# Optimization experiments

Hardware: AMD Instinct MI355X
Metric: run time of the kernel (lower is better)

Reference implementation:

```python
import jax, jax.numpy as jnp
from jax import lax
import numpy as np

B, H, W, C = 2, 128, 128, 256
HEADS, DH = 8, 32
HD = HEADS * DH  # must equal C (pos_emb reshape constraint)


def _lrelu(t):
    return jnp.where(t > 0, t, 0.01 * t)


def _mlp(t, w1, b1, w2):
    # Linear(dim->hd, bias) -> LeakyReLU -> Linear(hd->hd, no bias)
    return _lrelu(t @ w1.T + b1) @ w2.T


def _dwconv(t, w, b):
    # depthwise 3x3, padding 1; t: NCHW, w: (C,1,3,3)
    o = lax.conv_general_dilated(t, w, (1, 1), ((1, 1), (1, 1)),
                                 dimension_numbers=('NCHW', 'OIHW', 'NCHW'),
                                 feature_group_count=t.shape[1])
    return o + b[None, :, None, None]


def setup_inputs():
    key = jax.random.key(0)
    ks = iter(jax.random.split(key, 48))
    def nrm(shape, s=0.02):
        return jax.random.normal(next(ks), shape, jnp.float32) * s
    inp = {
        'x_in': jax.random.normal(next(ks), (B, H, W, C), jnp.float32),
        'y_in': jax.random.normal(next(ks), (B, H, W, C), jnp.float32),
        # fusion_x / fusion_y: two 1x1 convs (stored as (out,in) matrices)
        'fx_w1': nrm((C, 2 * C)), 'fx_b1': jnp.zeros((C,), jnp.float32),
        'fx_w2': nrm((C, C)),     'fx_b2': jnp.zeros((C,), jnp.float32),
        'fy_w1': nrm((C, 2 * C)), 'fy_b1': jnp.zeros((C,), jnp.float32),
        'fy_w2': nrm((C, C)),     'fy_b2': jnp.zeros((C,), jnp.float32),
        # to_q / to_k / to_v: Linear(C->HD,+b) -> LeakyReLU -> Linear(HD->HD, no b)
        'q_w1': nrm((HD, C)), 'q_b1': jnp.zeros((HD,), jnp.float32), 'q_w2': nrm((HD, HD)),
        'k_w1': nrm((HD, C)), 'k_b1': jnp.zeros((HD,), jnp.float32), 'k_w2': nrm((HD, HD)),
        'v_w1': nrm((HD, C)), 'v_b1': jnp.zeros((HD,), jnp.float32), 'v_w2': nrm((HD, HD)),
        'rescale_x': jnp.ones((HEADS, 1, 1), jnp.float32),
        'rescale_y': jnp.ones((HEADS, 1, 1), jnp.float32),
        'px_w': nrm((C, HD)), 'px_b': jnp.zeros((C,), jnp.float32),
        'py_w': nrm((C, HD)), 'py_b': jnp.zeros((C,), jnp.float32),
        # pos_emb: two depthwise 3x3 convs with GELU between
        'pe_w1': nrm((C, 1, 3, 3)), 'pe_b1': jnp.zeros((C,), jnp.float32),
        'pe_w2': nrm((C, 1, 3, 3)), 'pe_b2': jnp.zeros((C,), jnp.float32),
    }
    return inp


def reference(x_in, y_in, fx_w1, fx_b1, fx_w2, fx_b2, fy_w1, fy_b1, fy_w2, fy_b2,
              q_w1, q_b1, q_w2, k_w1, k_b1, k_w2, v_w1, v_b1, v_w2,
              rescale_x, rescale_y, px_w, px_b, py_w, py_b,
              pe_w1, pe_b1, pe_w2, pe_b2):
    b, h, w, c = x_in.shape
    n = h * w

    xy = jnp.concatenate([x_in, y_in], axis=-1)  # (b,h,w,2c)
    fk_x = _lrelu(jnp.einsum('bhwi,oi->bhwo', xy, fx_w1) + fx_b1)
    fk_x = (jnp.einsum('bhwi,oi->bhwo', fk_x, fx_w2) + fx_b2).reshape(b, n, c)
    fk_y = _lrelu(jnp.einsum('bhwi,oi->bhwo', xy, fy_w1) + fy_b1)
    fk_y = (jnp.einsum('bhwi,oi->bhwo', fk_y, fy_w2) + fy_b2).reshape(b, n, c)

    x = x_in.reshape(b, n, c)
    y = y_in.reshape(b, n, c)
    q_inp_x = _mlp(x, q_w1, q_b1, q_w2)
    k_inp_x = _mlp(fk_x, k_w1, k_b1, k_w2)
    v_inp_x = _mlp(x, v_w1, v_b1, v_w2)
    q_inp_y = _mlp(y, q_w1, q_b1, q_w2)
    k_inp_y = _mlp(fk_y, k_w1, k_b1, k_w2)
    v_inp_y = _mlp(y, v_w1, v_b1, v_w2)

    def split_heads(t):  # (b,n,hd) -> (b,heads,d,n)  (already transposed)
        return t.reshape(b, n, HEADS, DH).transpose(0, 2, 3, 1)

    def l2n(t):
        return t / jnp.maximum(jnp.linalg.norm(t, axis=-1, keepdims=True), 1e-12)

    q_x, k_x, v_x = split_heads(q_inp_x), split_heads(k_inp_x), split_heads(v_inp_x)
    q_y, k_y, v_y = split_heads(q_inp_y), split_heads(k_inp_y), split_heads(v_inp_y)
    q_x, k_x, q_y, k_y = l2n(q_x), l2n(k_x), l2n(q_y), l2n(k_y)

    def pos_emb(v_inp):
        t = v_inp.reshape(b, h, w, c).transpose(0, 3, 1, 2)  # NCHW
        t = _dwconv(t, pe_w1, pe_b1)
        t = jax.nn.gelu(t, approximate=False)
        t = _dwconv(t, pe_w2, pe_b2)
        return t.transpose(0, 2, 3, 1)  # NHWC

    # channel (transposed) cross-attention: d x d maps per head
    attn_x = jax.nn.softmax(jnp.einsum('bhdn,bhen->bhde', k_y, q_x) * rescale_x, axis=-1)
    xo = jnp.einsum('bhde,bhen->bhdn', attn_x, v_x).transpose(0, 3, 1, 2).reshape(b, n, HD)
    out_x = (xo @ px_w.T + px_b).reshape(b, h, w, c) + pos_emb(v_inp_x)

    attn_y = jax.nn.softmax(jnp.einsum('bhdn,bhen->bhde', k_x, q_y) * rescale_y, axis=-1)
    yo = jnp.einsum('bhde,bhen->bhdn', attn_y, v_y).transpose(0, 3, 1, 2).reshape(b, n, HD)
    out_y = (yo @ py_w.T + py_b).reshape(b, h, w, c) + pos_emb(v_inp_y)

    return out_x, out_y
```

## Files before the change

kernel.cpp:

```cpp
#include <hip/hip_runtime.h>
#include <hip/hip_bf16.h>

typedef __hip_bfloat16 bf16;
typedef __attribute__((ext_vector_type(8))) short short8;
typedef __attribute__((ext_vector_type(4))) short short4v;
typedef __attribute__((ext_vector_type(4))) float f32x4;

static __device__ __forceinline__ float bfbits2f(short s) {
    return __uint_as_float(((unsigned int)(unsigned short)s) << 16);
}
static __device__ __forceinline__ float bf2f(bf16 v) { return __bfloat162float(v); }
static __device__ __forceinline__ bf16 f2bf(float v) { return __float2bfloat16(v); }
static __device__ __forceinline__ short f2bfbits(float f) {
    bf16 h = __float2bfloat16(f);
    return *reinterpret_cast<short*>(&h);
}

__launch_bounds__(256)
__global__ void cvt_xy_kernel(const float* __restrict__ x, const float* __restrict__ y,
                              bf16* __restrict__ xb, bf16* __restrict__ yb)
{
    int t = blockIdx.x * 256 + threadIdx.x;
    int which = t >> 20;
    size_t i = (size_t)(t & 1048575) * 8;
    const float4* s = (const float4*)((which ? y : x) + i);
    float4 a = s[0], b = s[1];
    short8 p;
    p[0] = f2bfbits(a.x); p[1] = f2bfbits(a.y); p[2] = f2bfbits(a.z); p[3] = f2bfbits(a.w);
    p[4] = f2bfbits(b.x); p[5] = f2bfbits(b.y); p[6] = f2bfbits(b.z); p[7] = f2bfbits(b.w);
    *(short8*)((which ? yb : xb) + i) = p;
}

struct WTab {
    const float* src[10];
    bf16* dst[10];
    int nblk[10];
};

__launch_bounds__(256)
__global__ void cvt_w_kernel(WTab tab)
{
    int b = blockIdx.x;
    int a = 0, base = 0;
    while (a < 9 && b >= base + tab.nblk[a]) { base += tab.nblk[a]; ++a; }
    int lb = b - base;
    size_t i = ((size_t)lb * 256 + threadIdx.x) * 4;
    const float4 v = *(const float4*)(tab.src[a] + i);
    bf16* d = tab.dst[a] + i;
    d[0] = f2bf(v.x); d[1] = f2bf(v.y); d[2] = f2bf(v.z); d[3] = f2bf(v.w);
}

__launch_bounds__(256)
__global__ void cvt_pe_kernel(const float* __restrict__ w1, const float* __restrict__ w2,
                              float* __restrict__ t1, float* __restrict__ t2)
{
    int t = blockIdx.x * 256 + threadIdx.x;
    if (t >= 4608) return;
    int which = t >= 2304;
    int i = which ? t - 2304 : t;
    int c = i / 9, k = i % 9;
    (which ? t2 : t1)[k * 256 + c] = (which ? w2 : w1)[i];
}

template<int ROWS>
static __device__ __forceinline__ void stage8(const bf16* __restrict__ g, int ldk,
                                              char* dst, int tid, long r0, int k0)
{
#pragma unroll
    for (int r = 0; r < ROWS / 128; ++r) {
        int row = r * 128 + (tid >> 2);
        int q = (tid & 3) * 16;
        int srcq = q ^ (((row >> 1) & 3) << 4);
        const char* gsrc = (const char*)(g + (size_t)(r0 + row) * ldk + k0) + srcq;
        char* ldst = dst + r * 8192 + ((tid >> 6) << 10);
        __builtin_amdgcn_global_load_lds(
            (const __attribute__((address_space(1))) unsigned int*)gsrc,
            (__attribute__((address_space(3))) unsigned int*)ldst, 16, 0, 0);
    }
}

static __device__ __forceinline__ int h_off(int r, int c)
{
    return ((r * 264 + c) * 2) ^ (((r >> 2) & 3) << 4);
}

template<int K1, bool CONCAT, bool STAGE2, bool B2, bool TRANSOUT, bool PROJ>
__launch_bounds__(512)
__global__ void mlp_kernel(const bf16* __restrict__ A0, const bf16* __restrict__ A1,
                           const bf16* __restrict__ B1, const float* __restrict__ b1,
                           const bf16* __restrict__ W2, const float* __restrict__ b2v,
                           bf16* __restrict__ outb, bf16* __restrict__ outT,
                           float* __restrict__ outf, float* __restrict__ nrm)
{
    constexpr int LDS_SZ = STAGE2 ? 67584 : 49152;
    __shared__ __align__(16) char lds[LDS_SZ];
    int tid = threadIdx.x;
    int lane = tid & 63, wid = tid >> 6;
    int wr = wid >> 2, wc = wid & 3;
    long m0 = (long)blockIdx.y * 128;
    const bf16* Bp = B1;
    if (PROJ) Bp += (size_t)(m0 >> 14) * 65536;
    char* Abuf = lds;
    char* Bbuf = lds + 16384;

    f32x4 acc[4][4];
#pragma unroll
    for (int i = 0; i < 4; ++i)
#pragma unroll
        for (int j = 0; j < 4; ++j) acc[i][j] = (f32x4){0.f, 0.f, 0.f, 0.f};

    stage8<128>(A0, 256, Abuf, tid, m0, 0);
    stage8<256>(Bp, K1, Bbuf, tid, 0, 0);

    int kb = (lane >> 4) * 16;
    int offa[4], offb[4];
#pragma unroll
    for (int mi = 0; mi < 4; ++mi) {
        int row = wr * 64 + mi * 16 + (lane & 15);
        offa[mi] = row * 64 + (kb ^ (((row >> 1) & 3) << 4));
    }
#pragma unroll
    for (int ni = 0; ni < 4; ++ni) {
        int row = wc * 64 + ni * 16 + (lane & 15);
        offb[ni] = row * 64 + (kb ^ (((row >> 1) & 3) << 4));
    }

    constexpr int NT1 = K1 / 32;
    for (int kt = 0; kt < NT1; ++kt) {
        __syncthreads();
        int cur = kt & 1;
        if (kt + 1 < NT1) {
            int k0 = (kt + 1) * 32;
            const bf16* As = A0; int kk = k0;
            if (CONCAT && k0 >= 256) { As = A1; kk = k0 - 256; }
            stage8<128>(As, 256, Abuf + (cur ^ 1) * 8192, tid, m0, kk);
            stage8<256>(Bp, K1, Bbuf + (cur ^ 1) * 16384, tid, 0, k0);
        }
        const char* As = Abuf + cur * 8192;
        const char* Bs = Bbuf + cur * 16384;
        short8 af[4], bfr[4];
#pragma unroll
        for (int mi = 0; mi < 4; ++mi) af[mi] = *(const short8*)(As + offa[mi]);
#pragma unroll
        for (int ni = 0; ni < 4; ++ni) bfr[ni] = *(const short8*)(Bs + offb[ni]);
#pragma unroll
        for (int mi = 0; mi < 4; ++mi)
#pragma unroll
            for (int ni = 0; ni < 4; ++ni)
                acc[mi][ni] = __builtin_amdgcn_mfma_f32_16x16x32_bf16(af[mi], bfr[ni], acc[mi][ni], 0, 0, 0);
    }

    if constexpr (STAGE2) {
        float bv1[4];
#pragma unroll
        for (int ni = 0; ni < 4; ++ni) bv1[ni] = b1[wc * 64 + ni * 16 + (lane & 15)];
        __syncthreads();
#pragma unroll
        for (int mi = 0; mi < 4; ++mi)
#pragma unroll
            for (int ni = 0; ni < 4; ++ni) {
                int c = wc * 64 + ni * 16 + (lane & 15);
#pragma unroll
                for (int j = 0; j < 4; ++j) {
                    int r = wr * 64 + mi * 16 + (lane >> 4) * 4 + j;
                    float v = acc[mi][ni][j] + bv1[ni];
                    v = v > 0.f ? v : 0.01f * v;
                    *(bf16*)(lds + h_off(r, c)) = f2bf(v);
                }
            }
        __syncthreads();
        f32x4 acc2[4][4];
#pragma unroll
        for (int i = 0; i < 4; ++i)
#pragma unroll
            for (int j = 0; j < 4; ++j) acc2[i][j] = (f32x4){0.f, 0.f, 0.f, 0.f};
#pragma unroll
        for (int kc = 0; kc < 8; ++kc) {
            short8 af2[4], bf2[4];
#pragma unroll
            for (int mi = 0; mi < 4; ++mi) {
                int rm = wr * 64 + mi * 16 + (lane & 15);
                af2[mi] = *(const short8*)(lds + h_off(rm, kc * 32 + (lane >> 4) * 8));
            }
#pragma unroll
            for (int ni = 0; ni < 4; ++ni) {
                int ro = wc * 64 + ni * 16 + (lane & 15);
                bf2[ni] = *(const short8*)(W2 + ro * 256 + kc * 32 + (lane >> 4) * 8);
            }
#pragma unroll
            for (int mi = 0; mi < 4; ++mi)
#pragma unroll
                for (int ni = 0; ni < 4; ++ni)
                    acc2[mi][ni] = __builtin_amdgcn_mfma_f32_16x16x32_bf16(af2[mi], bf2[ni], acc2[mi][ni], 0, 0, 0);
        }
#pragma unroll
        for (int mi = 0; mi < 4; ++mi)
#pragma unroll
            for (int ni = 0; ni < 4; ++ni) acc[mi][ni] = acc2[mi][ni];
    }

    float bvo[4];
#pragma unroll
    for (int ni = 0; ni < 4; ++ni) {
        int col = wc * 64 + ni * 16 + (lane & 15);
        if (PROJ)            bvo[ni] = (m0 >= 32768 ? b2v : b1)[col];
        else if (B2)         bvo[ni] = b2v[col];
        else                 bvo[ni] = 0.f;
    }
    long r0 = m0 + wr * 64;
    float vsq[4] = {0.f, 0.f, 0.f, 0.f};
#pragma unroll
    for (int mi = 0; mi < 4; ++mi)
#pragma unroll
        for (int ni = 0; ni < 4; ++ni) {
            int col = wc * 64 + ni * 16 + (lane & 15);
            if (TRANSOUT) {
                short4v pk;
#pragma unroll
                for (int j = 0; j < 4; ++j) {
                    float v = acc[mi][ni][j];
                    vsq[ni] += v * v;
                    pk[j] = f2bfbits(v);
                }
                long row = r0 + mi * 16 + (lane >> 4) * 4;
                *(short4v*)(outT + (size_t)col * 65536 + row) = pk;
            } else {
#pragma unroll
                for (int j = 0; j < 4; ++j) {
                    size_t row = (size_t)(r0 + mi * 16 + (lane >> 4) * 4 + j);
                    float v = acc[mi][ni][j] + bvo[ni];
                    if (PROJ) outf[row * 256 + col] = v;
                    else      outb[row * 256 + col] = f2bf(v);
                }
            }
        }
    if constexpr (TRANSOUT) {
        __syncthreads();
        float* cs = (float*)lds;
        if (tid < 256) cs[tid] = 0.f;
        __syncthreads();
#pragma unroll
        for (int ni = 0; ni < 4; ++ni)
            atomicAdd(&cs[wc * 64 + ni * 16 + (lane & 15)], vsq[ni]);
        __syncthreads();
        if (tid < 256)
            atomicAdd(nrm + (int)(m0 >> 14) * 256 + tid, cs[tid]);
    }
}

__launch_bounds__(256)
__global__ void gram_mfma_kernel(const bf16* __restrict__ qT, const bf16* __restrict__ kT,
                                 float* __restrict__ gram)
{
    __shared__ float g[1024];
    int bid = blockIdx.x;
    int ns = bid & 15, h = (bid >> 4) & 7, b = (bid >> 7) & 1, pair = bid >> 8;
    int tid = threadIdx.x;
    int lane = tid & 63, w = tid >> 6;
    long krow = pair ? (long)b * 16384 : (long)(32768 + b * 16384);
    long qrow = pair ? (long)(32768 + b * 16384) : (long)b * 16384;
    long nb = (long)ns * 1024 + w * 256 + (lane >> 4) * 8;
    const bf16* Kp = kT + krow + nb;
    const bf16* Qp = qT + qrow + nb;
    int ch = h * 32 + (lane & 15);

    f32x4 acc[2][2];
#pragma unroll
    for (int i = 0; i < 2; ++i)
#pragma unroll
        for (int j = 0; j < 2; ++j) acc[i][j] = (f32x4){0.f, 0.f, 0.f, 0.f};

    for (int it = 0; it < 8; ++it) {
        short8 af[2], bfr[2];
#pragma unroll
        for (int mi = 0; mi < 2; ++mi)
            af[mi] = *(const short8*)(Kp + (size_t)(ch + mi * 16) * 65536 + it * 32);
#pragma unroll
        for (int ni = 0; ni < 2; ++ni)
            bfr[ni] = *(const short8*)(Qp + (size_t)(ch + ni * 16) * 65536 + it * 32);
#pragma unroll
        for (int mi = 0; mi < 2; ++mi)
#pragma unroll
            for (int ni = 0; ni < 2; ++ni)
                acc[mi][ni] = __builtin_amdgcn_mfma_f32_16x16x32_bf16(af[mi], bfr[ni], acc[mi][ni], 0, 0, 0);
    }

#pragma unroll
    for (int k = 0; k < 4; ++k) g[tid + k * 256] = 0.f;
    __syncthreads();
#pragma unroll
    for (int mi = 0; mi < 2; ++mi)
#pragma unroll
        for (int ni = 0; ni < 2; ++ni) {
            int e = ni * 16 + (lane & 15);
#pragma unroll
            for (int j = 0; j < 4; ++j) {
                int d = mi * 16 + (lane >> 4) * 4 + j;
                atomicAdd(&g[d * 32 + e], acc[mi][ni][j]);
            }
        }
    __syncthreads();
    float* gp = gram + ((size_t)((pair * 2 + b) * 8 + h)) * 1024;
#pragma unroll
    for (int k = 0; k < 4; ++k)
        atomicAdd(gp + tid + k * 256, g[tid + k * 256]);
}

__launch_bounds__(256)
__global__ void attn_pw_kernel(const float* __restrict__ gram, const float* __restrict__ norm2,
                               const float* __restrict__ rsx, const float* __restrict__ rsy,
                               const float* __restrict__ pxw, const float* __restrict__ pyw,
                               bf16* __restrict__ PW)
{
    int bid = blockIdx.x;
    int h = bid & 7, b = (bid >> 3) & 1, pair = bid >> 4;
    const float* G = gram + ((size_t)((pair * 2 + b) * 8 + h)) * 1024;
    const float* nk2 = norm2 + (pair ? (4 + b) : (6 + b)) * 256 + h * 32;
    const float* nq2 = norm2 + (pair ? (2 + b) : (0 + b)) * 256 + h * 32;
    float rs = (pair ? rsy : rsx)[h];
    __shared__ float attn[32][32];
    int t = threadIdx.x;
    if (t < 32) {
        int d = t;
        float nk = fmaxf(sqrtf(nk2[d]), 1e-12f);
        float row[32];
        float mx = -3.4e38f;
#pragma unroll
        for (int e = 0; e < 32; ++e) {
            float nq = fmaxf(sqrtf(nq2[e]), 1e-12f);
            float L = G[d * 32 + e] / (nk * nq) * rs;
            row[e] = L;
            mx = fmaxf(mx, L);
        }
        float sum = 0.f;
#pragma unroll
        for (int e = 0; e < 32; ++e) { row[e] = expf(row[e] - mx); sum += row[e]; }
        float inv = 1.0f / sum;
#pragma unroll
        for (int e = 0; e < 32; ++e) attn[d][e] = row[e] * inv;
    }
    __syncthreads();
    const float* pw = pair ? pyw : pxw;
    int o = t;
    float wrow[32];
#pragma unroll
    for (int d2 = 0; d2 < 32; ++d2) wrow[d2] = pw[o * 256 + h * 32 + d2];
    bf16* dst = PW + ((size_t)(pair * 2 + b) * 256 + o) * 256 + h * 32;
#pragma unroll
    for (int e = 0; e < 32; ++e) {
        float sv = 0.f;
#pragma unroll
        for (int d2 = 0; d2 < 32; ++d2) sv += wrow[d2] * attn[d2][e];
        dst[e] = f2bf(sv);
    }
}

template<bool GELU_OUT_BF>
__launch_bounds__(256)
__global__ void dwconv_kernel(const bf16* __restrict__ in, const float* __restrict__ wT,
                              const float* __restrict__ bias, bf16* __restrict__ outb,
                              float* __restrict__ outf)
{
    int t = blockIdx.x * 256 + threadIdx.x;
    int cg = t & 31;
    int x = (t >> 5) & 127;
    int chunk = (t >> 12) & 31;
    int b = t >> 17;
    int c0 = cg * 8;

    float w[9][8];
#pragma unroll
    for (int k = 0; k < 9; ++k) {
        float4 a = *(const float4*)(wT + k * 256 + c0);
        float4 bq = *(const float4*)(wT + k * 256 + c0 + 4);
        w[k][0] = a.x; w[k][1] = a.y; w[k][2] = a.z; w[k][3] = a.w;
        w[k][4] = bq.x; w[k][5] = bq.y; w[k][6] = bq.z; w[k][7] = bq.w;
    }
    float bs[8];
    {
        float4 a = *(const float4*)(bias + c0);
        float4 bq = *(const float4*)(bias + c0 + 4);
        bs[0] = a.x; bs[1] = a.y; bs[2] = a.z; bs[3] = a.w;
        bs[4] = bq.x; bs[5] = bq.y; bs[6] = bq.z; bs[7] = bq.w;
    }
    const short8 z = (short8){0, 0, 0, 0, 0, 0, 0, 0};
    bool xm = x > 0, xp = x < 127;
    int y0 = chunk * 4;

    for (int yi = 0; yi < 4; ++yi) {
        int y = y0 + yi;
        float acc[8];
#pragma unroll
        for (int j = 0; j < 8; ++j) acc[j] = bs[j];
#pragma unroll
        for (int ky = -1; ky <= 1; ++ky) {
            int yy = y + ky;
            if (yy < 0 || yy > 127) continue;
            const bf16* rp = in + ((((size_t)b << 14) + (yy << 7) + x) << 8) + c0;
            short8 vm = xm ? *(const short8*)(rp - 256) : z;
            short8 vc = *(const short8*)(rp);
            short8 vp = xp ? *(const short8*)(rp + 256) : z;
            int k0 = (ky + 1) * 3;
#pragma unroll
            for (int j = 0; j < 8; ++j) {
                acc[j] += w[k0 + 0][j] * bfbits2f(vm[j]);
                acc[j] += w[k0 + 1][j] * bfbits2f(vc[j]);
                acc[j] += w[k0 + 2][j] * bfbits2f(vp[j]);
            }
        }
        size_t base = ((((size_t)b << 14) + (y << 7) + x) << 8) + c0;
        if (GELU_OUT_BF) {
            short8 p;
#pragma unroll
            for (int j = 0; j < 8; ++j) {
                float a = acc[j];
                a = 0.5f * a * (1.0f + erff(a * 0.70710678118654752f));
                p[j] = f2bfbits(a);
            }
            *(short8*)(outb + base) = p;
        } else {
            float4* o = (float4*)(outf + base);
            float4 o0 = o[0], o1 = o[1];
            o0.x += acc[0]; o0.y += acc[1]; o0.z += acc[2]; o0.w += acc[3];
            o1.x += acc[4]; o1.y += acc[5]; o1.z += acc[6]; o1.w += acc[7];
            o[0] = o0; o[1] = o1;
        }
    }
}

extern "C" void kernel_launch(void* const* d_in, const int* in_sizes, int n_in,
                              void* d_out, int out_size, void* d_ws, size_t ws_size,
                              hipStream_t stream)
{
    const float* x_in  = (const float*)d_in[0];
    const float* y_in  = (const float*)d_in[1];
    const float* fx_w1 = (const float*)d_in[2];
    const float* fx_b1 = (const float*)d_in[3];
    const float* fx_w2 = (const float*)d_in[4];
    const float* fx_b2 = (const float*)d_in[5];
    const float* fy_w1 = (const float*)d_in[6];
    const float* fy_b1 = (const float*)d_in[7];
    const float* fy_w2 = (const float*)d_in[8];
    const float* fy_b2 = (const float*)d_in[9];
    const float* q_w1  = (const float*)d_in[10];
    const float* q_b1  = (const float*)d_in[11];
    const float* q_w2  = (const float*)d_in[12];
    const float* k_w1  = (const float*)d_in[13];
    const float* k_b1  = (const float*)d_in[14];
    const float* k_w2  = (const float*)d_in[15];
    const float* v_w1  = (const float*)d_in[16];
    const float* v_b1  = (const float*)d_in[17];
    const float* v_w2  = (const float*)d_in[18];
    const float* rescale_x = (const float*)d_in[19];
    const float* rescale_y = (const float*)d_in[20];
    const float* px_w  = (const float*)d_in[21];
    const float* px_b  = (const float*)d_in[22];
    const float* py_w  = (const float*)d_in[23];
    const float* py_b  = (const float*)d_in[24];
    const float* pe_w1 = (const float*)d_in[25];
    const float* pe_b1 = (const float*)d_in[26];
    const float* pe_w2 = (const float*)d_in[27];
    const float* pe_b2 = (const float*)d_in[28];

    char* ws = (char*)d_ws;
    const size_t NB = 16777216;
    bf16* xbf  = (bf16*)(ws + 0 * NB);
    bf16* ybf  = (bf16*)(ws + 1 * NB);
    bf16* fkx  = (bf16*)(ws + 2 * NB);
    bf16* fky  = (bf16*)(ws + 3 * NB);
    bf16* vbuf = (bf16*)(ws + 4 * NB);
    bf16* qT   = (bf16*)(ws + 6 * NB);
    bf16* kT   = (bf16*)(ws + 8 * NB);
    char* wreg = ws + 10 * NB;
    bf16* w_fx1 = (bf16*)(wreg + 0);
    bf16* w_fx2 = (bf16*)(wreg + 262144);
    bf16* w_fy1 = (bf16*)(wreg + 393216);
    bf16* w_fy2 = (bf16*)(wreg + 655360);
    bf16* w_q1  = (bf16*)(wreg + 786432);
    bf16* w_q2  = (bf16*)(wreg + 917504);
    bf16* w_k1  = (bf16*)(wreg + 1048576);
    bf16* w_k2  = (bf16*)(wreg + 1179648);
    bf16* w_v1  = (bf16*)(wreg + 1310720);
    bf16* w_v2  = (bf16*)(wreg + 1441792);
    float* gram  = (float*)(wreg + 1572864);
    float* norm2 = (float*)(wreg + 1572864 + 131072);
    bf16* PW     = (bf16*)(wreg + 1572864 + 139264);
    float* peT1  = (float*)(wreg + 1572864 + 139264 + 524288);
    float* peT2  = (float*)(wreg + 1572864 + 139264 + 524288 + 9216);
    bf16* ctmp   = (bf16*)(ws + 2 * NB);

    float* outx = (float*)d_out;
    float* outy = outx + 8388608;

    hipMemsetAsync(gram, 0, 139264, stream);

    cvt_xy_kernel<<<8192, 256, 0, stream>>>(x_in, y_in, xbf, ybf);
    WTab tab;
    const float* ws_src[10] = {fx_w1, fx_w2, fy_w1, fy_w2, q_w1, q_w2, k_w1, k_w2, v_w1, v_w2};
    bf16* ws_dst[10] = {w_fx1, w_fx2, w_fy1, w_fy2, w_q1, w_q2, w_k1, w_k2, w_v1, w_v2};
    int nblk[10] = {128, 64, 128, 64, 64, 64, 64, 64, 64, 64};
    for (int i = 0; i < 10; ++i) { tab.src[i] = ws_src[i]; tab.dst[i] = ws_dst[i]; tab.nblk[i] = nblk[i]; }
    cvt_w_kernel<<<768, 256, 0, stream>>>(tab);
    cvt_pe_kernel<<<18, 256, 0, stream>>>(pe_w1, pe_w2, peT1, peT2);

    dim3 g256(1, 256), g512(1, 512);
    mlp_kernel<512, true,  true,  true,  false, false><<<g256, 512, 0, stream>>>(
        xbf, ybf, w_fx1, fx_b1, w_fx2, fx_b2, fkx, nullptr, nullptr, nullptr);
    mlp_kernel<512, true,  true,  true,  false, false><<<g256, 512, 0, stream>>>(
        xbf, ybf, w_fy1, fy_b1, w_fy2, fy_b2, fky, nullptr, nullptr, nullptr);
    mlp_kernel<256, false, true,  false, true,  false><<<g512, 512, 0, stream>>>(
        xbf, nullptr, w_q1, q_b1, w_q2, nullptr, nullptr, qT, nullptr, norm2);
    mlp_kernel<256, false, true,  false, false, false><<<g512, 512, 0, stream>>>(
        xbf, nullptr, w_v1, v_b1, w_v2, nullptr, vbuf, nullptr, nullptr, nullptr);
    mlp_kernel<256, false, true,  false, true,  false><<<g512, 512, 0, stream>>>(
        fkx, nullptr, w_k1, k_b1, w_k2, nullptr, nullptr, kT, nullptr, norm2 + 1024);

    gram_mfma_kernel<<<512, 256, 0, stream>>>(qT, kT, gram);
    attn_pw_kernel<<<32, 256, 0, stream>>>(gram, norm2, rescale_x, rescale_y, px_w, py_w, PW);

    mlp_kernel<256, false, false, false, false, true><<<g512, 512, 0, stream>>>(
        vbuf, nullptr, PW, px_b, nullptr, py_b, nullptr, nullptr, outx, nullptr);

    dwconv_kernel<true ><<<1024, 256, 0, stream>>>(vbuf, peT1, pe_b1, ctmp, nullptr);
    dwconv_kernel<false><<<1024, 256, 0, stream>>>(ctmp, peT2, pe_b2, nullptr, outx);
    dwconv_kernel<true ><<<1024, 256, 0, stream>>>(vbuf + (size_t)32768 * 256, peT1, pe_b1, ctmp, nullptr);
    dwconv_kernel<false><<<1024, 256, 0, stream>>>(ctmp, peT2, pe_b2, nullptr, outy);
}
```

Baseline: 475.7 us.

## Merge prep kernels, batch paired MLPs per launch, restructure MLP stage-2 and epilogues

Folds the three conversion kernels and the gram memset into one prep launch. Pairs the two fusion MLPs and the q/v MLPs into single launches selected by blockIdx.x, and batches the two dwconv passes across both streams. Stage 2 of the MLP now has each wave own 32 output columns across all 128 rows, with double-buffered W2 register loads. Outputs are staged through swizzled LDS so global stores are coalesced 16-byte writes, including the transposed q/k output. The projection moves to its own kernel and the first dwconv is moved earlier in the schedule. The aim is fewer launches, better occupancy and coalesced stores, at the cost of a second ctmp buffer and higher register pressure under the new launch bounds.

```diff
diff --git a/kernel.cpp b/kernel.cpp
--- a/kernel.cpp
+++ b/kernel.cpp
@@ -3,7 +3,6 @@
 
 typedef __hip_bfloat16 bf16;
 typedef __attribute__((ext_vector_type(8))) short short8;
-typedef __attribute__((ext_vector_type(4))) short short4v;
 typedef __attribute__((ext_vector_type(4))) float f32x4;
 
 static __device__ __forceinline__ float bfbits2f(short s) {
@@ -16,50 +15,47 @@
     return *reinterpret_cast<short*>(&h);
 }
 
+struct PrepArgs {
+    const float *x, *y; bf16 *xb, *yb;
+    const float* wsrc[10]; bf16* wdst[10]; int wblk[10];
+    const float *pw1, *pw2; float *t1, *t2;
+    float4* zero;
+};
+
 __launch_bounds__(256)
-__global__ void cvt_xy_kernel(const float* __restrict__ x, const float* __restrict__ y,
-                              bf16* __restrict__ xb, bf16* __restrict__ yb)
-{
-    int t = blockIdx.x * 256 + threadIdx.x;
-    int which = t >> 20;
-    size_t i = (size_t)(t & 1048575) * 8;
-    const float4* s = (const float4*)((which ? y : x) + i);
-    float4 a = s[0], b = s[1];
-    short8 p;
-    p[0] = f2bfbits(a.x); p[1] = f2bfbits(a.y); p[2] = f2bfbits(a.z); p[3] = f2bfbits(a.w);
-    p[4] = f2bfbits(b.x); p[5] = f2bfbits(b.y); p[6] = f2bfbits(b.z); p[7] = f2bfbits(b.w);
-    *(short8*)((which ? yb : xb) + i) = p;
-}
-
-struct WTab {
-    const float* src[10];
-    bf16* dst[10];
-    int nblk[10];
-};
-
-__launch_bounds__(256)
-__global__ void cvt_w_kernel(WTab tab)
-{
-    int b = blockIdx.x;
-    int a = 0, base = 0;
-    while (a < 9 && b >= base + tab.nblk[a]) { base += tab.nblk[a]; ++a; }
-    int lb = b - base;
-    size_t i = ((size_t)lb * 256 + threadIdx.x) * 4;
-    const float4 v = *(const float4*)(tab.src[a] + i);
-    bf16* d = tab.dst[a] + i;
-    d[0] = f2bf(v.x); d[1] = f2bf(v.y); d[2] = f2bf(v.z); d[3] = f2bf(v.w);
-}
-
-__launch_bounds__(256)
-__global__ void cvt_pe_kernel(const float* __restrict__ w1, const float* __restrict__ w2,
-                              float* __restrict__ t1, float* __restrict__ t2)
-{
-    int t = blockIdx.x * 256 + threadIdx.x;
-    if (t >= 4608) return;
-    int which = t >= 2304;
-    int i = which ? t - 2304 : t;
-    int c = i / 9, k = i % 9;
-    (which ? t2 : t1)[k * 256 + c] = (which ? w2 : w1)[i];
+__global__ void prep_kernel(PrepArgs a)
+{
+    int blk = blockIdx.x, tid = threadIdx.x;
+    if (blk < 8192) {
+        int t = blk * 256 + tid;
+        int which = t >> 20;
+        size_t i = (size_t)(t & 1048575) * 8;
+        const float4* s = (const float4*)((which ? a.y : a.x) + i);
+        float4 u = s[0], v = s[1];
+        short8 p;
+        p[0] = f2bfbits(u.x); p[1] = f2bfbits(u.y); p[2] = f2bfbits(u.z); p[3] = f2bfbits(u.w);
+        p[4] = f2bfbits(v.x); p[5] = f2bfbits(v.y); p[6] = f2bfbits(v.z); p[7] = f2bfbits(v.w);
+        *(short8*)((which ? a.yb : a.xb) + i) = p;
+    } else if (blk < 8960) {
+        int b = blk - 8192;
+        int ai = 0, base = 0;
+        while (ai < 9 && b >= base + a.wblk[ai]) { base += a.wblk[ai]; ++ai; }
+        size_t i = ((size_t)(b - base) * 256 + tid) * 4;
+        const float4 v = *(const float4*)(a.wsrc[ai] + i);
+        bf16* d = a.wdst[ai] + i;
+        d[0] = f2bf(v.x); d[1] = f2bf(v.y); d[2] = f2bf(v.z); d[3] = f2bf(v.w);
+    } else if (blk < 8978) {
+        int t = (blk - 8960) * 256 + tid;
+        if (t < 4608) {
+            int which = t >= 2304;
+            int i = which ? t - 2304 : t;
+            int c = i / 9, k = i % 9;
+            (which ? a.t2 : a.t1)[k * 256 + c] = (which ? a.pw2 : a.pw1)[i];
+        }
+    } else {
+        int i = (blk - 8978) * 256 + tid;
+        a.zero[i] = make_float4(0.f, 0.f, 0.f, 0.f);
+    }
 }
 
 template<int ROWS>
@@ -79,27 +75,31 @@
     }
 }
 
-static __device__ __forceinline__ int h_off(int r, int c)
-{
-    return ((r * 264 + c) * 2) ^ (((r >> 2) & 3) << 4);
-}
-
-template<int K1, bool CONCAT, bool STAGE2, bool B2, bool TRANSOUT, bool PROJ>
-__launch_bounds__(512)
+static __device__ __forceinline__ int h_off2(int r, int c)
+{
+    return r * 512 + ((c * 2) ^ ((r & 7) << 4));
+}
+
+struct MlpArgs {
+    const bf16* B1[2]; const float* b1[2];
+    const bf16* W2[2]; const float* b2[2];
+    bf16* outb[2]; bf16* outT[2]; float* nrm[2];
+};
+
+template<int K1, bool CONCAT, bool B2OUT, bool TRANS0>
+__launch_bounds__(512, 4)
 __global__ void mlp_kernel(const bf16* __restrict__ A0, const bf16* __restrict__ A1,
-                           const bf16* __restrict__ B1, const float* __restrict__ b1,
-                           const bf16* __restrict__ W2, const float* __restrict__ b2v,
-                           bf16* __restrict__ outb, bf16* __restrict__ outT,
-                           float* __restrict__ outf, float* __restrict__ nrm)
-{
-    constexpr int LDS_SZ = STAGE2 ? 67584 : 49152;
-    __shared__ __align__(16) char lds[LDS_SZ];
+                           MlpArgs args)
+{
+    __shared__ __align__(16) char lds[66560];
     int tid = threadIdx.x;
     int lane = tid & 63, wid = tid >> 6;
+    int c16 = lane & 15, kg = lane >> 4;
     int wr = wid >> 2, wc = wid & 3;
+    int sel = blockIdx.x;
     long m0 = (long)blockIdx.y * 128;
-    const bf16* Bp = B1;
-    if (PROJ) Bp += (size_t)(m0 >> 14) * 65536;
+    const bf16* B1p = args.B1[sel];
+    const bf16* W2p = args.W2[sel];
     char* Abuf = lds;
     char* Bbuf = lds + 16384;
 
@@ -110,18 +110,18 @@
         for (int j = 0; j < 4; ++j) acc[i][j] = (f32x4){0.f, 0.f, 0.f, 0.f};
 
     stage8<128>(A0, 256, Abuf, tid, m0, 0);
-    stage8<256>(Bp, K1, Bbuf, tid, 0, 0);
-
-    int kb = (lane >> 4) * 16;
+    stage8<256>(B1p, K1, Bbuf, tid, 0, 0);
+
+    int kb = kg * 16;
     int offa[4], offb[4];
 #pragma unroll
     for (int mi = 0; mi < 4; ++mi) {
-        int row = wr * 64 + mi * 16 + (lane & 15);
+        int row = wr * 64 + mi * 16 + c16;
         offa[mi] = row * 64 + (kb ^ (((row >> 1) & 3) << 4));
     }
 #pragma unroll
     for (int ni = 0; ni < 4; ++ni) {
-        int row = wc * 64 + ni * 16 + (lane & 15);
+        int row = wc * 64 + ni * 16 + c16;
         offb[ni] = row * 64 + (kb ^ (((row >> 1) & 3) << 4));
     }
 
@@ -134,7 +134,7 @@
             const bf16* As = A0; int kk = k0;
             if (CONCAT && k0 >= 256) { As = A1; kk = k0 - 256; }
             stage8<128>(As, 256, Abuf + (cur ^ 1) * 8192, tid, m0, kk);
-            stage8<256>(Bp, K1, Bbuf + (cur ^ 1) * 16384, tid, 0, k0);
+            stage8<256>(B1p, K1, Bbuf + (cur ^ 1) * 16384, tid, 0, k0);
         }
         const char* As = Abuf + cur * 8192;
         const char* Bs = Bbuf + cur * 16384;
@@ -150,102 +150,188 @@
                 acc[mi][ni] = __builtin_amdgcn_mfma_f32_16x16x32_bf16(af[mi], bfr[ni], acc[mi][ni], 0, 0, 0);
     }
 
-    if constexpr (STAGE2) {
-        float bv1[4];
-#pragma unroll
-        for (int ni = 0; ni < 4; ++ni) bv1[ni] = b1[wc * 64 + ni * 16 + (lane & 15)];
-        __syncthreads();
-#pragma unroll
-        for (int mi = 0; mi < 4; ++mi)
-#pragma unroll
-            for (int ni = 0; ni < 4; ++ni) {
-                int c = wc * 64 + ni * 16 + (lane & 15);
+    int co0 = wid * 32 + c16;
+    short8 wf[2][2];
+    wf[0][0] = *(const short8*)(W2p + (size_t)co0 * 256 + kg * 8);
+    wf[0][1] = *(const short8*)(W2p + (size_t)(co0 + 16) * 256 + kg * 8);
+
+    float bv1[4];
+#pragma unroll
+    for (int ni = 0; ni < 4; ++ni) bv1[ni] = args.b1[sel][wc * 64 + ni * 16 + c16];
+    __syncthreads();
+#pragma unroll
+    for (int mi = 0; mi < 4; ++mi)
+#pragma unroll
+        for (int ni = 0; ni < 4; ++ni) {
+            int c = wc * 64 + ni * 16 + c16;
+#pragma unroll
+            for (int j = 0; j < 4; ++j) {
+                int r = wr * 64 + mi * 16 + kg * 4 + j;
+                float v = acc[mi][ni][j] + bv1[ni];
+                v = v > 0.f ? v : 0.01f * v;
+                *(bf16*)(lds + h_off2(r, c)) = f2bf(v);
+            }
+        }
+    __syncthreads();
+
+    f32x4 acc2[8][2];
+#pragma unroll
+    for (int i = 0; i < 8; ++i) {
+        acc2[i][0] = (f32x4){0.f, 0.f, 0.f, 0.f};
+        acc2[i][1] = (f32x4){0.f, 0.f, 0.f, 0.f};
+    }
+    for (int kc = 0; kc < 8; ++kc) {
+        int cur = kc & 1;
+        if (kc < 7) {
+            wf[cur ^ 1][0] = *(const short8*)(W2p + (size_t)co0 * 256 + (kc + 1) * 32 + kg * 8);
+            wf[cur ^ 1][1] = *(const short8*)(W2p + (size_t)(co0 + 16) * 256 + (kc + 1) * 32 + kg * 8);
+        }
+#pragma unroll
+        for (int mi = 0; mi < 8; ++mi) {
+            short8 a2 = *(const short8*)(lds + h_off2(mi * 16 + c16, kc * 32 + kg * 8));
+            acc2[mi][0] = __builtin_amdgcn_mfma_f32_16x16x32_bf16(a2, wf[cur][0], acc2[mi][0], 0, 0, 0);
+            acc2[mi][1] = __builtin_amdgcn_mfma_f32_16x16x32_bf16(a2, wf[cur][1], acc2[mi][1], 0, 0, 0);
+        }
+    }
+
+    bool trans = TRANS0 && (sel == 0);
+    float vsq[2] = {0.f, 0.f};
+    __syncthreads();
+    if (trans) {
+#pragma unroll
+        for (int mi = 0; mi < 8; ++mi)
+#pragma unroll
+            for (int j2 = 0; j2 < 2; ++j2) {
+                int col = co0 + j2 * 16;
 #pragma unroll
                 for (int j = 0; j < 4; ++j) {
-                    int r = wr * 64 + mi * 16 + (lane >> 4) * 4 + j;
-                    float v = acc[mi][ni][j] + bv1[ni];
-                    v = v > 0.f ? v : 0.01f * v;
-                    *(bf16*)(lds + h_off(r, c)) = f2bf(v);
+                    float v = acc2[mi][j2][j];
+                    vsq[j2] += v * v;
+                    int row = mi * 16 + kg * 4 + j;
+                    *(bf16*)(lds + col * 256 + ((row * 2) ^ ((col & 7) << 4))) = f2bf(v);
                 }
             }
-        __syncthreads();
-        f32x4 acc2[4][4];
-#pragma unroll
-        for (int i = 0; i < 4; ++i)
-#pragma unroll
-            for (int j = 0; j < 4; ++j) acc2[i][j] = (f32x4){0.f, 0.f, 0.f, 0.f};
-#pragma unroll
-        for (int kc = 0; kc < 8; ++kc) {
-            short8 af2[4], bf2[4];
-#pragma unroll
-            for (int mi = 0; mi < 4; ++mi) {
-                int rm = wr * 64 + mi * 16 + (lane & 15);
-                af2[mi] = *(const short8*)(lds + h_off(rm, kc * 32 + (lane >> 4) * 8));
-            }
-#pragma unroll
-            for (int ni = 0; ni < 4; ++ni) {
-                int ro = wc * 64 + ni * 16 + (lane & 15);
-                bf2[ni] = *(const short8*)(W2 + ro * 256 + kc * 32 + (lane >> 4) * 8);
-            }
-#pragma unroll
-            for (int mi = 0; mi < 4; ++mi)
-#pragma unroll
-                for (int ni = 0; ni < 4; ++ni)
-                    acc2[mi][ni] = __builtin_amdgcn_mfma_f32_16x16x32_bf16(af2[mi], bf2[ni], acc2[mi][ni], 0, 0, 0);
-        }
-#pragma unroll
-        for (int mi = 0; mi < 4; ++mi)
-#pragma unroll
-            for (int ni = 0; ni < 4; ++ni) acc[mi][ni] = acc2[mi][ni];
-    }
-
-    float bvo[4];
-#pragma unroll
-    for (int ni = 0; ni < 4; ++ni) {
-        int col = wc * 64 + ni * 16 + (lane & 15);
-        if (PROJ)            bvo[ni] = (m0 >= 32768 ? b2v : b1)[col];
-        else if (B2)         bvo[ni] = b2v[col];
-        else                 bvo[ni] = 0.f;
-    }
-    long r0 = m0 + wr * 64;
-    float vsq[4] = {0.f, 0.f, 0.f, 0.f};
-#pragma unroll
-    for (int mi = 0; mi < 4; ++mi)
-#pragma unroll
-        for (int ni = 0; ni < 4; ++ni) {
-            int col = wc * 64 + ni * 16 + (lane & 15);
-            if (TRANSOUT) {
-                short4v pk;
+    } else {
+        float bvo[2];
+        bvo[0] = B2OUT ? args.b2[sel][co0] : 0.f;
+        bvo[1] = B2OUT ? args.b2[sel][co0 + 16] : 0.f;
+#pragma unroll
+        for (int mi = 0; mi < 8; ++mi)
+#pragma unroll
+            for (int j2 = 0; j2 < 2; ++j2) {
+                int col = co0 + j2 * 16;
 #pragma unroll
                 for (int j = 0; j < 4; ++j) {
-                    float v = acc[mi][ni][j];
-                    vsq[ni] += v * v;
-                    pk[j] = f2bfbits(v);
-                }
-                long row = r0 + mi * 16 + (lane >> 4) * 4;
-                *(short4v*)(outT + (size_t)col * 65536 + row) = pk;
-            } else {
-#pragma unroll
-                for (int j = 0; j < 4; ++j) {
-                    size_t row = (size_t)(r0 + mi * 16 + (lane >> 4) * 4 + j);
-                    float v = acc[mi][ni][j] + bvo[ni];
-                    if (PROJ) outf[row * 256 + col] = v;
-                    else      outb[row * 256 + col] = f2bf(v);
+                    int row = mi * 16 + kg * 4 + j;
+                    *(bf16*)(lds + h_off2(row, col)) = f2bf(acc2[mi][j2][j] + bvo[j2]);
                 }
             }
-        }
-    if constexpr (TRANSOUT) {
-        __syncthreads();
-        float* cs = (float*)lds;
+    }
+    __syncthreads();
+    if (trans) {
+        bf16* dst = args.outT[sel];
+#pragma unroll
+        for (int i = 0; i < 8; ++i) {
+            int g = i * 512 + tid;
+            int col = g >> 4, rc = g & 15;
+            short8 vv = *(const short8*)(lds + col * 256 + ((rc ^ (col & 7)) << 4));
+            *(short8*)(dst + (size_t)col * 65536 + m0 + rc * 8) = vv;
+        }
+        float* cs = (float*)(lds + 65536);
         if (tid < 256) cs[tid] = 0.f;
         __syncthreads();
-#pragma unroll
-        for (int ni = 0; ni < 4; ++ni)
-            atomicAdd(&cs[wc * 64 + ni * 16 + (lane & 15)], vsq[ni]);
+        atomicAdd(&cs[co0], vsq[0]);
+        atomicAdd(&cs[co0 + 16], vsq[1]);
         __syncthreads();
         if (tid < 256)
-            atomicAdd(nrm + (int)(m0 >> 14) * 256 + tid, cs[tid]);
-    }
+            atomicAdd(args.nrm[sel] + (int)(m0 >> 14) * 256 + tid, cs[tid]);
+    } else {
+        bf16* dst = args.outb[sel];
+#pragma unroll
+        for (int i = 0; i < 8; ++i) {
+            int g = i * 512 + tid;
+            int row = g >> 5, cc = g & 31;
+            short8 vv = *(const short8*)(lds + row * 512 + ((cc ^ (row & 7)) << 4));
+            *(short8*)(dst + (size_t)(m0 + row) * 256 + cc * 8) = vv;
+        }
+    }
+}
+
+__launch_bounds__(512, 6)
+__global__ void proj_kernel(const bf16* __restrict__ A0, const bf16* __restrict__ Bw,
+                            const float* __restrict__ bx, const float* __restrict__ by,
+                            float* __restrict__ outf)
+{
+    __shared__ __align__(16) char lds[49152];
+    int tid = threadIdx.x;
+    int lane = tid & 63, wid = tid >> 6;
+    int c16 = lane & 15, kg = lane >> 4;
+    int wr = wid >> 2, wc = wid & 3;
+    long m0 = (long)blockIdx.y * 128;
+    const bf16* Bp = Bw + (size_t)(m0 >> 14) * 65536;
+    char* Abuf = lds;
+    char* Bbuf = lds + 16384;
+
+    f32x4 acc[4][4];
+#pragma unroll
+    for (int i = 0; i < 4; ++i)
+#pragma unroll
+        for (int j = 0; j < 4; ++j) acc[i][j] = (f32x4){0.f, 0.f, 0.f, 0.f};
+
+    stage8<128>(A0, 256, Abuf, tid, m0, 0);
+    stage8<256>(Bp, 256, Bbuf, tid, 0, 0);
+
+    int kb = kg * 16;
+    int offa[4], offb[4];
+#pragma unroll
+    for (int mi = 0; mi < 4; ++mi) {
+        int row = wr * 64 + mi * 16 + c16;
+        offa[mi] = row * 64 + (kb ^ (((row >> 1) & 3) << 4));
+    }
+#pragma unroll
+    for (int ni = 0; ni < 4; ++ni) {
+        int row = wc * 64 + ni * 16 + c16;
+        offb[ni] = row * 64 + (kb ^ (((row >> 1) & 3) << 4));
+    }
+
+    for (int kt = 0; kt < 8; ++kt) {
+        __syncthreads();
+        int cur = kt & 1;
+        if (kt + 1 < 8) {
+            int k0 = (kt + 1) * 32;
+            stage8<128>(A0, 256, Abuf + (cur ^ 1) * 8192, tid, m0, k0);
+            stage8<256>(Bp, 256, Bbuf + (cur ^ 1) * 16384, tid, 0, k0);
+        }
+        const char* As = Abuf + cur * 8192;
+        const char* Bs = Bbuf + cur * 16384;
+        short8 af[4], bfr[4];
+#pragma unroll
+        for (int mi = 0; mi < 4; ++mi) af[mi] = *(const short8*)(As + offa[mi]);
+#pragma unroll
+        for (int ni = 0; ni < 4; ++ni) bfr[ni] = *(const short8*)(Bs + offb[ni]);
+#pragma unroll
+        for (int mi = 0; mi < 4; ++mi)
+#pragma unroll
+            for (int ni = 0; ni < 4; ++ni)
+                acc[mi][ni] = __builtin_amdgcn_mfma_f32_16x16x32_bf16(af[mi], bfr[ni], acc[mi][ni], 0, 0, 0);
+    }
+
+    const float* bsel = (m0 >= 32768) ? by : bx;
+    float bv[4];
+#pragma unroll
+    for (int ni = 0; ni < 4; ++ni) bv[ni] = bsel[wc * 64 + ni * 16 + c16];
+    long r0 = m0 + wr * 64;
+#pragma unroll
+    for (int mi = 0; mi < 4; ++mi)
+#pragma unroll
+        for (int ni = 0; ni < 4; ++ni) {
+            int col = wc * 64 + ni * 16 + c16;
+#pragma unroll
+            for (int j = 0; j < 4; ++j) {
+                size_t row = (size_t)(r0 + mi * 16 + kg * 4 + j);
+                outf[row * 256 + col] = acc[mi][ni][j] + bv[ni];
+            }
+        }
 }
 
 __launch_bounds__(256)
@@ -357,11 +443,17 @@
 
 template<bool GELU_OUT_BF>
 __launch_bounds__(256)
-__global__ void dwconv_kernel(const bf16* __restrict__ in, const float* __restrict__ wT,
-                              const float* __restrict__ bias, bf16* __restrict__ outb,
-                              float* __restrict__ outf)
-{
-    int t = blockIdx.x * 256 + threadIdx.x;
+__global__ void dwconv_kernel(const bf16* __restrict__ in0, const bf16* __restrict__ in1,
+                              const float* __restrict__ wT, const float* __restrict__ bias,
+                              bf16* __restrict__ ob0, bf16* __restrict__ ob1,
+                              float* __restrict__ of0, float* __restrict__ of1)
+{
+    int blk = blockIdx.x;
+    int sel = blk >> 10;
+    const bf16* in = sel ? in1 : in0;
+    bf16* outb = sel ? ob1 : ob0;
+    float* outf = sel ? of1 : of0;
+    int t = (blk & 1023) * 256 + threadIdx.x;
     int cg = t & 31;
     int x = (t >> 5) & 127;
     int chunk = (t >> 12) & 31;
@@ -487,42 +579,48 @@
     bf16* PW     = (bf16*)(wreg + 1572864 + 139264);
     float* peT1  = (float*)(wreg + 1572864 + 139264 + 524288);
     float* peT2  = (float*)(wreg + 1572864 + 139264 + 524288 + 9216);
-    bf16* ctmp   = (bf16*)(ws + 2 * NB);
+    bf16* ctmp1  = (bf16*)(ws + 2 * NB);
+    bf16* ctmp2  = (bf16*)(ws + 3 * NB);
 
     float* outx = (float*)d_out;
     float* outy = outx + 8388608;
 
-    hipMemsetAsync(gram, 0, 139264, stream);
-
-    cvt_xy_kernel<<<8192, 256, 0, stream>>>(x_in, y_in, xbf, ybf);
-    WTab tab;
+    PrepArgs pa;
+    pa.x = x_in; pa.y = y_in; pa.xb = xbf; pa.yb = ybf;
     const float* ws_src[10] = {fx_w1, fx_w2, fy_w1, fy_w2, q_w1, q_w2, k_w1, k_w2, v_w1, v_w2};
     bf16* ws_dst[10] = {w_fx1, w_fx2, w_fy1, w_fy2, w_q1, w_q2, w_k1, w_k2, w_v1, w_v2};
     int nblk[10] = {128, 64, 128, 64, 64, 64, 64, 64, 64, 64};
-    for (int i = 0; i < 10; ++i) { tab.src[i] = ws_src[i]; tab.dst[i] = ws_dst[i]; tab.nblk[i] = nblk[i]; }
-    cvt_w_kernel<<<768, 256, 0, stream>>>(tab);
-    cvt_pe_kernel<<<18, 256, 0, stream>>>(pe_w1, pe_w2, peT1, peT2);
-
-    dim3 g256(1, 256), g512(1, 512);
-    mlp_kernel<512, true,  true,  true,  false, false><<<g256, 512, 0, stream>>>(
-        xbf, ybf, w_fx1, fx_b1, w_fx2, fx_b2, fkx, nullptr, nullptr, nullptr);
-    mlp_kernel<512, true,  true,  true,  false, false><<<g256, 512, 0, stream>>>(
-        xbf, ybf, w_fy1, fy_b1, w_fy2, fy_b2, fky, nullptr, nullptr, nullptr);
-    mlp_kernel<256, false, true,  false, true,  false><<<g512, 512, 0, stream>>>(
-        xbf, nullptr, w_q1, q_b1, w_q2, nullptr, nullptr, qT, nullptr, norm2);
-    mlp_kernel<256, false, true,  false, false, false><<<g512, 512, 0, stream>>>(
-        xbf, nullptr, w_v1, v_b1, w_v2, nullptr, vbuf, nullptr, nullptr, nullptr);
-    mlp_kernel<256, false, true,  false, true,  false><<<g512, 512, 0, stream>>>(
-        fkx, nullptr, w_k1, k_b1, w_k2, nullptr, nullptr, kT, nullptr, norm2 + 1024);
+    for (int i = 0; i < 10; ++i) { pa.wsrc[i] = ws_src[i]; pa.wdst[i] = ws_dst[i]; pa.wblk[i] = nblk[i]; }
+    pa.pw1 = pe_w1; pa.pw2 = pe_w2; pa.t1 = peT1; pa.t2 = peT2;
+    pa.zero = (float4*)gram;
+    prep_kernel<<<9012, 256, 0, stream>>>(pa);
+
+    MlpArgs fa = {};
+    fa.B1[0] = w_fx1; fa.B1[1] = w_fy1; fa.b1[0] = fx_b1; fa.b1[1] = fy_b1;
+    fa.W2[0] = w_fx2; fa.W2[1] = w_fy2; fa.b2[0] = fx_b2; fa.b2[1] = fy_b2;
+    fa.outb[0] = fkx; fa.outb[1] = fky;
+    mlp_kernel<512, true, true, false><<<dim3(2, 256), 512, 0, stream>>>(xbf, ybf, fa);
+
+    MlpArgs qa = {};
+    qa.B1[0] = w_q1; qa.B1[1] = w_v1; qa.b1[0] = q_b1; qa.b1[1] = v_b1;
+    qa.W2[0] = w_q2; qa.W2[1] = w_v2;
+    qa.outT[0] = qT; qa.nrm[0] = norm2;
+    qa.outb[1] = vbuf;
+    mlp_kernel<256, false, false, true><<<dim3(2, 512), 512, 0, stream>>>(xbf, nullptr, qa);
+
+    MlpArgs ka = {};
+    ka.B1[0] = w_k1; ka.b1[0] = k_b1; ka.W2[0] = w_k2;
+    ka.outT[0] = kT; ka.nrm[0] = norm2 + 1024;
+    mlp_kernel<256, false, false, true><<<dim3(1, 512), 512, 0, stream>>>(fkx, nullptr, ka);
+
+    dwconv_kernel<true><<<2048, 256, 0, stream>>>(vbuf, vbuf + (size_t)32768 * 256,
+                                                  peT1, pe_b1, ctmp1, ctmp2, nullptr, nullptr);
 
     gram_mfma_kernel<<<512, 256, 0, stream>>>(qT, kT, gram);
     attn_pw_kernel<<<32, 256, 0, stream>>>(gram, norm2, rescale_x, rescale_y, px_w, py_w, PW);
 
-    mlp_kernel<256, false, false, false, false, true><<<g512, 512, 0, stream>>>(
-        vbuf, nullptr, PW, px_b, nullptr, py_b, nullptr, nullptr, outx, nullptr);
-
-    dwconv_kernel<true ><<<1024, 256, 0, stream>>>(vbuf, peT1, pe_b1, ctmp, nullptr);
-    dwconv_kernel<false><<<1024, 256, 0, stream>>>(ctmp, peT2, pe_b2, nullptr, outx);
-    dwconv_kernel<true ><<<1024, 256, 0, stream>>>(vbuf + (size_t)32768 * 256, peT1, pe_b1, ctmp, nullptr);
-    dwconv_kernel<false><<<1024, 256, 0, stream>>>(ctmp, peT2, pe_b2, nullptr, outy);
-}
+    proj_kernel<<<dim3(1, 512), 512, 0, stream>>>(vbuf, PW, px_b, py_b, outx);
+
+    dwconv_kernel<false><<<2048, 256, 0, stream>>>(ctmp1, ctmp2, peT2, pe_b2,
+                                                   nullptr, nullptr, outx, outy);
+}
```

Result: faster. 443.8 us (-6.7%).
